# Optimization experiments

Hardware: AMD Instinct MI355X
Metric: run time of the kernel (lower is better)

The kernel has to match this reference:

```python
import jax, jax.numpy as jnp
import numpy as np

DK, DV, NH = 512, 256, 8  # matches init_kwargs


def rel_to_abs(x):
    # x: (B, N, L, 2L-1) -> (B, N, L, L) via pad/reshape trick
    B, N, L, _ = x.shape
    x = jnp.pad(x, ((0, 0), (0, 0), (0, 0), (0, 1)))          # (B,N,L,2L)
    x = x.reshape(B, N, L * 2 * L)
    x = jnp.pad(x, ((0, 0), (0, 0), (0, L - 1)))
    x = x.reshape(B, N, L + 1, 2 * L - 1)
    return x[:, :, :L, L - 1:]


def relative_logits_1d(q, rel_k):
    # q: (B, nh, A, Wd, dkh); rel_k: (dkh, 2*Wd-1)
    B, nh, A, Wd, _ = q.shape
    rel = jnp.einsum('bnawc,cm->bnawm', q, rel_k)             # (B,nh,A,Wd,2Wd-1)
    rel = rel.reshape(B, nh * A, Wd, 2 * Wd - 1)
    rel = rel_to_abs(rel).reshape(B, nh, A, 1, Wd, Wd)
    return jnp.broadcast_to(rel, (B, nh, A, A, Wd, Wd))


def reference(x, w_qkv, w_conv, w_out, key_rel_h, key_rel_w):
    B, Cin, H, W = x.shape
    dkh, dvh = DK // NH, DV // NH
    L = H * W
    # 1x1 qkv projection (stride 1)
    qkv = jnp.einsum('bchw,oc->bohw', x, w_qkv)               # (B, 2dk+dv, H, W)
    q = qkv[:, :DK]
    k = qkv[:, DK:2 * DK]
    v = qkv[:, 2 * DK:]
    flat_q = q.reshape(B, NH, dkh, L) * (dkh ** -0.5)
    flat_k = k.reshape(B, NH, dkh, L)
    flat_v = v.reshape(B, NH, dvh, L)
    logits = jnp.einsum('bncs,bnct->bnst', flat_q, flat_k)     # (B,nh,L,L)
    # relative position logits (uses the already-scaled q, as in the torch code)
    qr = flat_q.reshape(B, NH, dkh, H, W).transpose(0, 1, 3, 4, 2)  # (B,nh,H,W,dkh)
    w_rel = relative_logits_1d(qr, key_rel_w)                  # (B,nh,H,H,W,W)
    h_rel = relative_logits_1d(qr.transpose(0, 1, 3, 2, 4), key_rel_h)  # (B,nh,W,W,H,H)
    h_rel = h_rel.transpose(0, 1, 2, 4, 3, 5).reshape(B, NH, L, L)
    w_rel = w_rel.transpose(0, 1, 4, 2, 5, 3).reshape(B, NH, L, L)
    logits = logits + h_rel + w_rel
    weights = jax.nn.softmax(logits, axis=-1)
    attn = jnp.einsum('bnst,bnct->bnsc', weights, flat_v)      # (B,nh,L,dvh)
    attn = attn.transpose(0, 1, 3, 2).reshape(B, DV, H, W)
    attn = jnp.einsum('bchw,oc->bohw', attn, w_out)            # 1x1 out_proj
    conv_out = jax.lax.conv_general_dilated(
        x, w_conv, window_strides=(1, 1), padding=[(1, 1), (1, 1)],
        dimension_numbers=('NCHW', 'OIHW', 'NCHW'))            # (B, out_c-dv, H, W)
    return jnp.concatenate([conv_out, attn], axis=1)


def setup_inputs() -> dict:
    key = jax.random.key(0)
    ks = jax.random.split(key, 6)
    H, W, Cin = 32, 32, 256
    return {
        'x': jax.random.normal(ks[0], (8, Cin, H, W), jnp.float32),
        'w_qkv': jax.random.normal(ks[1], (2 * DK + DV, Cin), jnp.float32) * 0.02,
        'w_conv': jax.random.normal(ks[2], (256, Cin, 3, 3), jnp.float32) * 0.02,
        'w_out': jax.random.normal(ks[3], (DV, DV), jnp.float32) * 0.02,
        'key_rel_h': DK ** -0.5 + jax.random.normal(ks[4], (DK // NH, 2 * H - 1), jnp.float32),
        'key_rel_w': DK ** -0.5 + jax.random.normal(ks[5], (DK // NH, 2 * W - 1), jnp.float32),
    }
```

## Files before the change

kernel.cpp:

```cpp
#include <hip/hip_runtime.h>
#include <cstddef>
#include <cstdint>

#define NB 8
#define CIN 256
#define LL 1024
#define DKC 512
#define DVC 256
#define XPSTRIDE 295936

typedef short short8 __attribute__((ext_vector_type(8)));
typedef float f32x4 __attribute__((ext_vector_type(4)));

__device__ __forceinline__ unsigned short f2bf(float f) {
  unsigned int u = __float_as_uint(f);
  u += 0x7fffu + ((u >> 16) & 1u);
  return (unsigned short)(u >> 16);
}
__device__ __forceinline__ float bf2f(unsigned short u) {
  return __uint_as_float(((unsigned int)u) << 16);
}

__global__ __launch_bounds__(256) void prep_all(
    const float* __restrict__ x, const float* __restrict__ wconv,
    const float* __restrict__ wqkv, const float* __restrict__ wout,
    const float* __restrict__ krh, const float* __restrict__ krw,
    unsigned short* __restrict__ wtap, unsigned short* __restrict__ wqbf,
    unsigned short* __restrict__ woutbf, unsigned short* __restrict__ relTh,
    unsigned short* __restrict__ relTw, unsigned short* __restrict__ xTp) {
  __shared__ float tile[64][65];
  const int tid = threadIdx.x;
  if (blockIdx.x < 128) {
    const int st = blockIdx.x & 15;
    const int b = blockIdx.x >> 4;
    const int s0 = st * 64;
    const int h0 = st * 2;
    for (int cc = 0; cc < 4; ++cc) {
      const int c0 = cc * 64;
      {
        const int row = tid >> 2;
        const int j0 = (tid & 3) * 16;
#pragma unroll
        for (int k = 0; k < 4; ++k)
          *(float4*)&tile[row][j0 + k * 4] =
              *(const float4*)(x + ((size_t)(b * CIN + c0 + row)) * LL + s0 + j0 + k * 4);
      }
      __syncthreads();
      {
        const int sl = tid >> 2;
        const int cb = (tid & 3) * 16;
        unsigned short buf[16];
#pragma unroll
        for (int m = 0; m < 16; ++m) buf[m] = f2bf(tile[cb + m][sl]);
        const int hp = h0 + (sl >> 5) + 1;
        const int wp = (sl & 31) + 1;
        unsigned short* dst = xTp + (size_t)b * XPSTRIDE + (hp * 34 + wp) * 256 + c0 + cb;
        *(uint4*)dst = *(uint4*)&buf[0];
        *(uint4*)(dst + 8) = *(uint4*)&buf[8];
      }
      __syncthreads();
    }
    return;
  }
  const int idx = (blockIdx.x - 128) * 256 + tid;
  if (idx < 589824) {
    const int g = idx >> 14;
    const int ot = g / 9, tap = g - ot * 9;
    const int rem2 = idx & 16383;
    const int kc = rem2 >> 12;
    const int row = (rem2 >> 6) & 63, kin = rem2 & 63;
    const int o = ot * 64 + row, c = kc * 64 + kin;
    wtap[idx] = f2bf(wconv[(size_t)(o * 256 + c) * 9 + tap]);
  } else if (idx < 917504) {
    const int j = idx - 589824;
    const int g = j >> 12;
    const int ot = g >> 2, kc = g & 3;
    const int row = (j >> 6) & 63, kin = j & 63;
    const int o = ot * 64 + row, c = kc * 64 + kin;
    const float sc = (o < DKC) ? 0.125f * 1.44269504088896f : 1.0f;
    wqbf[j] = f2bf(wqkv[o * 256 + c] * sc);
  } else if (idx < 983040) {
    const int j = idx - 917504;
    const int g = j >> 12;
    const int o = (g >> 2) * 64 + ((j >> 6) & 63);
    const int c = (g & 3) * 64 + (j & 63);
    woutbf[j] = f2bf(wout[o * 256 + c]);
  } else if (idx < 991232) {
    const int j = idx - 983040;
    const int tbl = j >> 12;
    const int rest = j & 4095;
    const int m = rest >> 6, c = rest & 63;
    const float* src = tbl ? krw : krh;
    unsigned short* dst = tbl ? relTw : relTh;
    const float v = (m < 63) ? src[c * 63 + m] : 0.f;
    dst[m * 64 + c] = f2bf(v);
  } else {
    const int j2 = idx - 991232;
    const int b = j2 / 33792;
    const int rem = j2 - b * 33792;
    const int pos = rem >> 8, c = rem & 255;
    int hp, wp;
    if (pos < 34) { hp = 0; wp = pos; }
    else if (pos < 68) { hp = 33; wp = pos - 34; }
    else if (pos < 100) { hp = pos - 68 + 1; wp = 0; }
    else { hp = pos - 100 + 1; wp = 33; }
    xTp[(size_t)b * XPSTRIDE + (hp * 34 + wp) * 256 + c] = 0;
  }
}

__global__ __launch_bounds__(256) void qkv_mfma(
    const unsigned short* __restrict__ xTp, const unsigned short* __restrict__ wqbf,
    unsigned short* __restrict__ qbf, unsigned short* __restrict__ kbf,
    unsigned short* __restrict__ vbf) {
  __shared__ __align__(16) char qsmem[16640];
  unsigned short* bs = (unsigned short*)qsmem;
  float (*trans)[65] = (float(*)[65])qsmem;
  const int tid = threadIdx.x;
  const int lane = tid & 63, w = tid >> 6;
  const int n16 = lane & 15, quad = lane >> 4;
  const int ot = blockIdx.x;
  const int st = blockIdx.y;
  const int b = blockIdx.z;
  const int s0 = st * 64;
  const int h0 = st * 2;
  const int trow = tid >> 3, ck = tid & 7;

  const unsigned short* xb = xTp + (size_t)b * XPSTRIDE;
  const unsigned short* wA = wqbf + (size_t)ot * 16384 + (w * 16 + n16) * 64 + quad * 8;
  const int wpos = (trow & 31) + 1;

  f32x4 acc[4];
#pragma unroll
  for (int nt = 0; nt < 4; ++nt) acc[nt] = (f32x4){0.f, 0.f, 0.f, 0.f};

  uint4 rb0 = *(const uint4*)(xb + (size_t)((h0 + 1) * 34 + wpos) * 256 + ck * 8);
  uint4 rb1 = *(const uint4*)(xb + (size_t)((h0 + 2) * 34 + wpos) * 256 + ck * 8);
  short8 af0 = *(const short8*)(wA);
  short8 af1 = *(const short8*)(wA + 32);
#pragma unroll
  for (int kc = 0; kc < 4; ++kc) {
    __syncthreads();
    *(uint4*)&bs[trow * 64 + ((ck ^ (trow & 7)) * 8)] = rb0;
    *(uint4*)&bs[(trow + 32) * 64 + ((ck ^ (trow & 7)) * 8)] = rb1;
    __syncthreads();
    short8 a0 = af0, a1 = af1;
    if (kc < 3) {
      const int c0 = (kc + 1) * 64;
      rb0 = *(const uint4*)(xb + (size_t)((h0 + 1) * 34 + wpos) * 256 + c0 + ck * 8);
      rb1 = *(const uint4*)(xb + (size_t)((h0 + 2) * 34 + wpos) * 256 + c0 + ck * 8);
      af0 = *(const short8*)(wA + (kc + 1) * 4096);
      af1 = *(const short8*)(wA + (kc + 1) * 4096 + 32);
    }
#pragma unroll
    for (int nt = 0; nt < 4; ++nt) {
      short8 b0 = *(const short8*)&bs[(nt * 16 + n16) * 64 + ((quad ^ (n16 & 7)) * 8)];
      short8 b1 = *(const short8*)&bs[(nt * 16 + n16) * 64 + (((quad + 4) ^ (n16 & 7)) * 8)];
      acc[nt] = __builtin_amdgcn_mfma_f32_16x16x32_bf16(a0, b0, acc[nt], 0, 0, 0);
      acc[nt] = __builtin_amdgcn_mfma_f32_16x16x32_bf16(a1, b1, acc[nt], 0, 0, 0);
    }
  }
  __syncthreads();
#pragma unroll
  for (int nt = 0; nt < 4; ++nt)
#pragma unroll
    for (int reg = 0; reg < 4; ++reg)
      trans[w * 16 + quad * 4 + reg][nt * 16 + n16] = acc[nt][reg];
  __syncthreads();
  const int sl = tid >> 2;
  const int cseg = (tid & 3) * 16;
  unsigned short buf[16];
  if (ot < 16) {
#pragma unroll
    for (int m = 0; m < 16; ++m) buf[m] = f2bf(trans[cseg + m][sl]);
    unsigned short* dst;
    int head;
    if (ot < 8) { dst = qbf; head = ot; }
    else { dst = kbf; head = ot - 8; }
    const size_t base = (((size_t)(b * 8 + head)) * LL + s0 + sl) * 64 + cseg;
    *(uint4*)(dst + base) = *(uint4*)&buf[0];
    *(uint4*)(dst + base + 8) = *(uint4*)&buf[8];
  } else {
#pragma unroll
    for (int m = 0; m < 16; ++m) buf[m] = f2bf(trans[sl][cseg + m]);
    unsigned short* dst = vbf + ((size_t)b * DVC + (ot - 16) * 64 + sl) * LL + s0 + cseg;
    *(uint4*)dst = *(uint4*)&buf[0];
    *(uint4*)(dst + 8) = *(uint4*)&buf[8];
  }
}

__global__ __launch_bounds__(256) void conv_mfma(
    const unsigned short* __restrict__ xTp, const unsigned short* __restrict__ wtap,
    float* __restrict__ out) {
  __shared__ __align__(16) unsigned short bs[64 * 64];
  const int tid = threadIdx.x;
  const int lane = tid & 63, w = tid >> 6;
  const int n16 = lane & 15, quad = lane >> 4;
  const int ot = blockIdx.x;
  const int st = blockIdx.y;
  const int b = blockIdx.z;
  const int s0 = st * 64;
  const int h0 = st * 2;
  const int trow = tid >> 3;
  const int ck = tid & 7;

  const unsigned short* xb = xTp + (size_t)b * XPSTRIDE;
  const unsigned short* wA = wtap + (size_t)ot * 147456 + (w * 16 + n16) * 64 + quad * 8;

  f32x4 acc[4];
#pragma unroll
  for (int nt = 0; nt < 4; ++nt) acc[nt] = (f32x4){0.f, 0.f, 0.f, 0.f};

  uint4 rb0, rb1;
  auto loadB = [&](int it) {
    const int tap = it >> 2;
    const int c0 = (it & 3) * 64;
    const int dh = tap / 3 - 1;
    const int dw = tap - (tap / 3) * 3 - 1;
    const int wp = (trow & 31) + dw + 1;
    rb0 = *(const uint4*)(xb + (size_t)((h0 + dh + 1) * 34 + wp) * 256 + c0 + ck * 8);
    rb1 = *(const uint4*)(xb + (size_t)((h0 + dh + 2) * 34 + wp) * 256 + c0 + ck * 8);
  };
  loadB(0);
  short8 af0 = *(const short8*)(wA);
  short8 af1 = *(const short8*)(wA + 32);
  for (int it = 0; it < 36; ++it) {
    __syncthreads();
    *(uint4*)&bs[trow * 64 + ((ck ^ (trow & 7)) * 8)] = rb0;
    *(uint4*)&bs[(trow + 32) * 64 + ((ck ^ (trow & 7)) * 8)] = rb1;
    __syncthreads();
    short8 a0 = af0, a1 = af1;
    if (it < 35) {
      loadB(it + 1);
      af0 = *(const short8*)(wA + (size_t)(it + 1) * 4096);
      af1 = *(const short8*)(wA + (size_t)(it + 1) * 4096 + 32);
    }
#pragma unroll
    for (int nt = 0; nt < 4; ++nt) {
      short8 b0 = *(const short8*)&bs[(nt * 16 + n16) * 64 + ((quad ^ (n16 & 7)) * 8)];
      short8 b1 = *(const short8*)&bs[(nt * 16 + n16) * 64 + (((quad + 4) ^ (n16 & 7)) * 8)];
      acc[nt] = __builtin_amdgcn_mfma_f32_16x16x32_bf16(a0, b0, acc[nt], 0, 0, 0);
      acc[nt] = __builtin_amdgcn_mfma_f32_16x16x32_bf16(a1, b1, acc[nt], 0, 0, 0);
    }
  }
#pragma unroll
  for (int nt = 0; nt < 4; ++nt)
#pragma unroll
    for (int reg = 0; reg < 4; ++reg)
      out[((size_t)b * 512 + ot * 64 + w * 16 + quad * 4 + reg) * LL + s0 + nt * 16 + n16] =
          acc[nt][reg];
}

__global__ __launch_bounds__(256, 2) void attn_kernel(
    const unsigned short* __restrict__ qbf, const unsigned short* __restrict__ kbf,
    const unsigned short* __restrict__ vbf, const unsigned short* __restrict__ relTh,
    const unsigned short* __restrict__ relTw, unsigned short* __restrict__ abf) {
  __shared__ __align__(16) char smem[45056];
  unsigned short* ks = (unsigned short*)smem;
  unsigned short* vs = (unsigned short*)(smem + 8192);
  unsigned short* ps = (unsigned short*)(smem + 12288);
  unsigned short* rwtT = (unsigned short*)(smem + 28672);
  float* obuf = (float*)smem;

  const int tid = threadIdx.x;
  const int lane = tid & 63, w = tid >> 6;
  const int n16 = lane & 15, quad = lane >> 4;
  const int blk = blockIdx.x;
  const int bn = blk & 63, qt = blk >> 6;
  const int n = bn & 7, b = bn >> 3;
  const int s0 = qt * 128;
  const int pb = (w & 1) * 16;
  const int aar[2] = {4 * qt + (w >> 1), 4 * qt + 2 + (w >> 1)};

  const unsigned short* qbase = qbf + ((size_t)(b * 8 + n)) * LL * 64;
  const unsigned short* kbase = kbf + ((size_t)(b * 8 + n)) * LL * 64;
  const unsigned short* vbase = vbf + ((size_t)(b * 8 + n)) * 32 * LL;

  const int ck = tid & 7;
  const int trow = tid >> 3;

  uint4 pk0 = *(const uint4*)(kbase + trow * 64 + ck * 8);
  uint4 pk1 = *(const uint4*)(kbase + (trow + 32) * 64 + ck * 8);
  uint4 pv = *(const uint4*)(vbase + (size_t)trow * LL + ck * 8);

#pragma unroll
  for (int rs = 0; rs < 2; ++rs) {
    const int aa = aar[rs];
    const int sT = (pb + n16) * 32 + aa;
    short8 ra0 = *(const short8*)(qbase + (size_t)sT * 64 + quad * 8);
    short8 ra1 = *(const short8*)(qbase + (size_t)sT * 64 + 32 + quad * 8);
#pragma unroll
    for (int tbl = 0; tbl < 2; ++tbl) {
      const unsigned short* rel = tbl ? relTh : relTw;
      f32x4 acc[4];
#pragma unroll
      for (int mt = 0; mt < 4; ++mt) acc[mt] = (f32x4){0.f, 0.f, 0.f, 0.f};
#pragma unroll
      for (int mt = 0; mt < 4; ++mt) {
        short8 b0 = *(const short8*)(rel + (mt * 16 + n16) * 64 + quad * 8);
        short8 b1 = *(const short8*)(rel + (mt * 16 + n16) * 64 + 32 + quad * 8);
        acc[mt] = __builtin_amdgcn_mfma_f32_16x16x32_bf16(ra0, b0, acc[mt], 0, 0, 0);
        acc[mt] = __builtin_amdgcn_mfma_f32_16x16x32_bf16(ra1, b1, acc[mt], 0, 0, 0);
      }
      if (tbl == 0) {
#pragma unroll
        for (int mt = 0; mt < 4; ++mt)
#pragma unroll
          for (int reg = 0; reg < 4; ++reg)
            rwtT[(mt * 16 + n16) * 128 +
                 ((rs * 64 + w * 16 + quad * 4 + reg) ^ ((n16 & 7) * 8))] = f2bf(acc[mt][reg]);
      } else {
#pragma unroll
        for (int mt = 0; mt < 4; ++mt)
#pragma unroll
          for (int reg = 0; reg < 4; ++reg)
            ps[(rs * 64 + w * 16 + quad * 4 + reg) * 64 + mt * 16 + n16] = f2bf(acc[mt][reg]);
      }
    }
  }
  short8 qf[2][2];
#pragma unroll
  for (int rs = 0; rs < 2; ++rs) {
    const size_t qrow = (size_t)(s0 + rs * 64 + w * 16 + n16) * 64;
    qf[rs][0] = *(const short8*)(qbase + qrow + quad * 8);
    qf[rs][1] = *(const short8*)(qbase + qrow + 32 + quad * 8);
  }
  __syncthreads();
  float rhreg[2][2][4];
#pragma unroll
  for (int rs = 0; rs < 2; ++rs)
#pragma unroll
    for (int tt1 = 0; tt1 < 2; ++tt1)
#pragma unroll
      for (int reg = 0; reg < 4; ++reg) {
        const int iL = quad * 4 + reg;
        rhreg[rs][tt1][reg] =
            bf2f(ps[(rs * 64 + w * 16 + iL) * 64 + tt1 * 16 + n16 + 31 - pb - iL]);
      }

  float lacc[2][4] = {};
  f32x4 oacc[2][2];
#pragma unroll
  for (int rs = 0; rs < 2; ++rs)
#pragma unroll
    for (int ct = 0; ct < 2; ++ct) oacc[rs][ct] = (f32x4){0.f, 0.f, 0.f, 0.f};

  const int rbq = w * 16 + quad * 4;

  for (int kt64 = 0; kt64 < 16; ++kt64) {
    const int t0 = kt64 * 64;
    __syncthreads();
    *(uint4*)&ks[trow * 64 + ((ck ^ (trow & 7)) * 8)] = pk0;
    *(uint4*)&ks[(trow + 32) * 64 + ((ck ^ (trow & 7)) * 8)] = pk1;
    *(uint4*)&vs[trow * 64 + ((ck ^ (trow & 7)) * 8)] = pv;
    __syncthreads();
    if (kt64 < 15) {
      const unsigned short* kg = kbase + (size_t)(t0 + 64) * 64;
      pk0 = *(const uint4*)(kg + trow * 64 + ck * 8);
      pk1 = *(const uint4*)(kg + (trow + 32) * 64 + ck * 8);
      pv = *(const uint4*)(vbase + (size_t)trow * LL + t0 + 64 + ck * 8);
    }

    f32x4 sacc[2][4];
#pragma unroll
    for (int rs = 0; rs < 2; ++rs)
#pragma unroll
      for (int tt = 0; tt < 4; ++tt) sacc[rs][tt] = (f32x4){0.f, 0.f, 0.f, 0.f};
#pragma unroll
    for (int tt = 0; tt < 4; ++tt) {
      short8 kb0 = *(const short8*)&ks[(tt * 16 + n16) * 64 + ((quad ^ (n16 & 7)) * 8)];
      short8 kb1 = *(const short8*)&ks[(tt * 16 + n16) * 64 + (((quad + 4) ^ (n16 & 7)) * 8)];
#pragma unroll
      for (int rs = 0; rs < 2; ++rs) {
        sacc[rs][tt] = __builtin_amdgcn_mfma_f32_16x16x32_bf16(qf[rs][0], kb0, sacc[rs][tt], 0, 0, 0);
        sacc[rs][tt] = __builtin_amdgcn_mfma_f32_16x16x32_bf16(qf[rs][1], kb1, sacc[rs][tt], 0, 0, 0);
      }
    }
    float rwv[2][2][4];
#pragma unroll
    for (int rs = 0; rs < 2; ++rs)
#pragma unroll
      for (int h = 0; h < 2; ++h) {
        const int mw = (t0 >> 5) + h - aar[rs] + 31;
        const ushort4 rw4 =
            *(const ushort4*)&rwtT[mw * 128 + ((rs * 64 + rbq) ^ ((mw & 7) * 8))];
        rwv[rs][h][0] = bf2f(rw4.x); rwv[rs][h][1] = bf2f(rw4.y);
        rwv[rs][h][2] = bf2f(rw4.z); rwv[rs][h][3] = bf2f(rw4.w);
      }
#pragma unroll
    for (int rs = 0; rs < 2; ++rs)
#pragma unroll
      for (int tt = 0; tt < 4; ++tt)
#pragma unroll
        for (int reg = 0; reg < 4; ++reg) {
          const float e = __builtin_amdgcn_exp2f(sacc[rs][tt][reg] + rwv[rs][tt >> 1][reg] +
                                                 rhreg[rs][tt & 1][reg]);
          lacc[rs][reg] += e;
          const int r = quad * 4 + reg;
          ps[(rs * 64 + w * 16 + r) * 64 + (((tt * 2 + (n16 >> 3)) ^ (r & 7)) * 8) + (n16 & 7)] =
              (unsigned short)(__float_as_uint(e) >> 16);
        }
    __asm__ volatile("s_waitcnt lgkmcnt(0)" ::: "memory");
#pragma unroll
    for (int kt = 0; kt < 2; ++kt) {
      short8 pa[2];
#pragma unroll
      for (int rs = 0; rs < 2; ++rs)
        pa[rs] = *(const short8*)&ps[(rs * 64 + w * 16 + n16) * 64 +
                                     (((quad + 4 * kt) ^ (n16 & 7)) * 8)];
#pragma unroll
      for (int ct = 0; ct < 2; ++ct) {
        short8 vb = *(const short8*)&vs[(ct * 16 + n16) * 64 + (((quad + 4 * kt) ^ (n16 & 7)) * 8)];
#pragma unroll
        for (int rs = 0; rs < 2; ++rs)
          oacc[rs][ct] = __builtin_amdgcn_mfma_f32_16x16x32_bf16(pa[rs], vb, oacc[rs][ct], 0, 0, 0);
      }
    }
  }
  float linv[2][4];
#pragma unroll
  for (int rs = 0; rs < 2; ++rs)
#pragma unroll
    for (int reg = 0; reg < 4; ++reg) {
      float l = lacc[rs][reg];
#pragma unroll
      for (int m = 1; m < 16; m <<= 1) l += __shfl_xor(l, m, 16);
      linv[rs][reg] = 1.0f / l;
    }
  __syncthreads();
#pragma unroll
  for (int rs = 0; rs < 2; ++rs)
#pragma unroll
    for (int ct = 0; ct < 2; ++ct)
#pragma unroll
      for (int reg = 0; reg < 4; ++reg)
        obuf[(rs * 64 + w * 16 + quad * 4 + reg) * 33 + ct * 16 + n16] =
            oacc[rs][ct][reg] * linv[rs][reg];
  __syncthreads();
  {
    const int row = tid >> 1;
    const int cseg = (tid & 1) * 16;
    unsigned short buf16[16];
#pragma unroll
    for (int m = 0; m < 16; ++m) buf16[m] = f2bf(obuf[row * 33 + cseg + m]);
    unsigned short* dst = abf + (((size_t)b * LL) + s0 + row) * 256 + n * 32 + cseg;
    *(uint4*)dst = *(uint4*)&buf16[0];
    *(uint4*)(dst + 8) = *(uint4*)&buf16[8];
  }
}

__global__ __launch_bounds__(256) void proj_mfma(
    const unsigned short* __restrict__ abf, const unsigned short* __restrict__ woutbf,
    float* __restrict__ out) {
  __shared__ __align__(16) unsigned short bs[64 * 64];
  const int tid = threadIdx.x;
  const int lane = tid & 63, w = tid >> 6;
  const int n16 = lane & 15, quad = lane >> 4;
  const int ot = blockIdx.x;
  const int st = blockIdx.y;
  const int b = blockIdx.z;
  const int s0 = st * 64;
  const int trow = tid >> 3, ck = tid & 7;

  const unsigned short* ab = abf + ((size_t)b * LL + s0) * 256;
  const unsigned short* wA = woutbf + (size_t)ot * 16384 + (w * 16 + n16) * 64 + quad * 8;

  f32x4 acc[4];
#pragma unroll
  for (int nt = 0; nt < 4; ++nt) acc[nt] = (f32x4){0.f, 0.f, 0.f, 0.f};

  uint4 rb0 = *(const uint4*)(ab + (size_t)trow * 256 + ck * 8);
  uint4 rb1 = *(const uint4*)(ab + (size_t)(trow + 32) * 256 + ck * 8);
  short8 af0 = *(const short8*)(wA);
  short8 af1 = *(const short8*)(wA + 32);
#pragma unroll
  for (int kc = 0; kc < 4; ++kc) {
    __syncthreads();
    *(uint4*)&bs[trow * 64 + ((ck ^ (trow & 7)) * 8)] = rb0;
    *(uint4*)&bs[(trow + 32) * 64 + ((ck ^ (trow & 7)) * 8)] = rb1;
    __syncthreads();
    short8 a0 = af0, a1 = af1;
    if (kc < 3) {
      const int c0 = (kc + 1) * 64;
      rb0 = *(const uint4*)(ab + (size_t)trow * 256 + c0 + ck * 8);
      rb1 = *(const uint4*)(ab + (size_t)(trow + 32) * 256 + c0 + ck * 8);
      af0 = *(const short8*)(wA + (kc + 1) * 4096);
      af1 = *(const short8*)(wA + (kc + 1) * 4096 + 32);
    }
#pragma unroll
    for (int nt = 0; nt < 4; ++nt) {
      short8 b0 = *(const short8*)&bs[(nt * 16 + n16) * 64 + ((quad ^ (n16 & 7)) * 8)];
      short8 b1 = *(const short8*)&bs[(nt * 16 + n16) * 64 + (((quad + 4) ^ (n16 & 7)) * 8)];
      acc[nt] = __builtin_amdgcn_mfma_f32_16x16x32_bf16(a0, b0, acc[nt], 0, 0, 0);
      acc[nt] = __builtin_amdgcn_mfma_f32_16x16x32_bf16(a1, b1, acc[nt], 0, 0, 0);
    }
  }
#pragma unroll
  for (int nt = 0; nt < 4; ++nt)
#pragma unroll
    for (int reg = 0; reg < 4; ++reg)
      out[((size_t)b * 512 + 256 + ot * 64 + w * 16 + quad * 4 + reg) * LL + s0 + nt * 16 + n16] =
          acc[nt][reg];
}

extern "C" void kernel_launch(void* const* d_in, const int* in_sizes, int n_in,
                              void* d_out, int out_size, void* d_ws, size_t ws_size,
                              hipStream_t stream) {
  const float* x     = (const float*)d_in[0];
  const float* wqkv  = (const float*)d_in[1];
  const float* wconv = (const float*)d_in[2];
  const float* wout  = (const float*)d_in[3];
  const float* krh   = (const float*)d_in[4];
  const float* krw   = (const float*)d_in[5];
  float* out = (float*)d_out;

  unsigned short* qbf = (unsigned short*)d_ws;
  unsigned short* kbf = qbf + (size_t)NB * 8 * LL * 64;
  unsigned short* vbf = kbf + (size_t)NB * 8 * LL * 64;
  unsigned short* abf = vbf + (size_t)NB * DVC * LL;
  unsigned short* relTh = abf + (size_t)NB * LL * DVC;
  unsigned short* relTw = relTh + 4096;
  unsigned short* xTp = relTw + 4096;
  unsigned short* wtap = xTp + (size_t)NB * XPSTRIDE;
  unsigned short* wqbf = wtap + 589824;
  unsigned short* woutbf = wqbf + 327680;

  prep_all<<<dim3(5056), 256, 0, stream>>>(x, wconv, wqkv, wout, krh, krw,
                                           wtap, wqbf, woutbf, relTh, relTw, xTp);
  qkv_mfma<<<dim3(20, 16, NB), 256, 0, stream>>>(xTp, wqbf, qbf, kbf, vbf);
  conv_mfma<<<dim3(4, 16, NB), 256, 0, stream>>>(xTp, wtap, out);
  attn_kernel<<<dim3(512), 256, 0, stream>>>(qbf, kbf, vbf, relTh, relTw, abf);
  proj_mfma<<<dim3(4, 16, NB), 256, 0, stream>>>(abf, woutbf, out);
}
```

Before: 161.8 us.

## Load GEMM B fragments directly from global into registers, drop LDS staging

In the qkv, conv and output-projection MFMA kernels, each lane now loads its B-operand fragments straight from global memory into registers, double-buffered across k-steps. This replaces the shared-memory tile and the two barriers per iteration. The aim is to remove LDS traffic and synchronisation so loads overlap with MFMAs. In exchange, each of the four waves fetches the same B data on its own, which raises global/L2 traffic fourfold and raises register pressure, especially in the fully unrolled 36-step conv loop.

```diff
diff --git a/kernel.cpp b/kernel.cpp
--- a/kernel.cpp
+++ b/kernel.cpp
@@ -112,9 +112,7 @@
     const unsigned short* __restrict__ xTp, const unsigned short* __restrict__ wqbf,
     unsigned short* __restrict__ qbf, unsigned short* __restrict__ kbf,
     unsigned short* __restrict__ vbf) {
-  __shared__ __align__(16) char qsmem[16640];
-  unsigned short* bs = (unsigned short*)qsmem;
-  float (*trans)[65] = (float(*)[65])qsmem;
+  __shared__ float trans[64][65];
   const int tid = threadIdx.x;
   const int lane = tid & 63, w = tid >> 6;
   const int n16 = lane & 15, quad = lane >> 4;
@@ -123,43 +121,51 @@
   const int b = blockIdx.z;
   const int s0 = st * 64;
   const int h0 = st * 2;
-  const int trow = tid >> 3, ck = tid & 7;
 
   const unsigned short* xb = xTp + (size_t)b * XPSTRIDE;
   const unsigned short* wA = wqbf + (size_t)ot * 16384 + (w * 16 + n16) * 64 + quad * 8;
-  const int wpos = (trow & 31) + 1;
+
+  const unsigned short* bp[4];
+#pragma unroll
+  for (int nt = 0; nt < 4; ++nt) {
+    const int sl2 = nt * 16 + n16;
+    const int hp = h0 + (sl2 >> 5) + 1;
+    const int wp = (sl2 & 31) + 1;
+    bp[nt] = xb + (size_t)(hp * 34 + wp) * 256 + quad * 8;
+  }
 
   f32x4 acc[4];
 #pragma unroll
   for (int nt = 0; nt < 4; ++nt) acc[nt] = (f32x4){0.f, 0.f, 0.f, 0.f};
 
-  uint4 rb0 = *(const uint4*)(xb + (size_t)((h0 + 1) * 34 + wpos) * 256 + ck * 8);
-  uint4 rb1 = *(const uint4*)(xb + (size_t)((h0 + 2) * 34 + wpos) * 256 + ck * 8);
-  short8 af0 = *(const short8*)(wA);
-  short8 af1 = *(const short8*)(wA + 32);
+  short8 bf[2][4][2];
+  short8 af[2][2];
+#pragma unroll
+  for (int nt = 0; nt < 4; ++nt) {
+    bf[0][nt][0] = *(const short8*)(bp[nt]);
+    bf[0][nt][1] = *(const short8*)(bp[nt] + 32);
+  }
+  af[0][0] = *(const short8*)(wA);
+  af[0][1] = *(const short8*)(wA + 32);
 #pragma unroll
   for (int kc = 0; kc < 4; ++kc) {
-    __syncthreads();
-    *(uint4*)&bs[trow * 64 + ((ck ^ (trow & 7)) * 8)] = rb0;
-    *(uint4*)&bs[(trow + 32) * 64 + ((ck ^ (trow & 7)) * 8)] = rb1;
-    __syncthreads();
-    short8 a0 = af0, a1 = af1;
+    const int cur = kc & 1, nxt = cur ^ 1;
     if (kc < 3) {
       const int c0 = (kc + 1) * 64;
-      rb0 = *(const uint4*)(xb + (size_t)((h0 + 1) * 34 + wpos) * 256 + c0 + ck * 8);
-      rb1 = *(const uint4*)(xb + (size_t)((h0 + 2) * 34 + wpos) * 256 + c0 + ck * 8);
-      af0 = *(const short8*)(wA + (kc + 1) * 4096);
-      af1 = *(const short8*)(wA + (kc + 1) * 4096 + 32);
+#pragma unroll
+      for (int nt = 0; nt < 4; ++nt) {
+        bf[nxt][nt][0] = *(const short8*)(bp[nt] + c0);
+        bf[nxt][nt][1] = *(const short8*)(bp[nt] + c0 + 32);
+      }
+      af[nxt][0] = *(const short8*)(wA + (kc + 1) * 4096);
+      af[nxt][1] = *(const short8*)(wA + (kc + 1) * 4096 + 32);
     }
 #pragma unroll
     for (int nt = 0; nt < 4; ++nt) {
-      short8 b0 = *(const short8*)&bs[(nt * 16 + n16) * 64 + ((quad ^ (n16 & 7)) * 8)];
-      short8 b1 = *(const short8*)&bs[(nt * 16 + n16) * 64 + (((quad + 4) ^ (n16 & 7)) * 8)];
-      acc[nt] = __builtin_amdgcn_mfma_f32_16x16x32_bf16(a0, b0, acc[nt], 0, 0, 0);
-      acc[nt] = __builtin_amdgcn_mfma_f32_16x16x32_bf16(a1, b1, acc[nt], 0, 0, 0);
-    }
-  }
-  __syncthreads();
+      acc[nt] = __builtin_amdgcn_mfma_f32_16x16x32_bf16(af[cur][0], bf[cur][nt][0], acc[nt], 0, 0, 0);
+      acc[nt] = __builtin_amdgcn_mfma_f32_16x16x32_bf16(af[cur][1], bf[cur][nt][1], acc[nt], 0, 0, 0);
+    }
+  }
 #pragma unroll
   for (int nt = 0; nt < 4; ++nt)
 #pragma unroll
@@ -191,7 +197,6 @@
 __global__ __launch_bounds__(256) void conv_mfma(
     const unsigned short* __restrict__ xTp, const unsigned short* __restrict__ wtap,
     float* __restrict__ out) {
-  __shared__ __align__(16) unsigned short bs[64 * 64];
   const int tid = threadIdx.x;
   const int lane = tid & 63, w = tid >> 6;
   const int n16 = lane & 15, quad = lane >> 4;
@@ -200,46 +205,57 @@
   const int b = blockIdx.z;
   const int s0 = st * 64;
   const int h0 = st * 2;
-  const int trow = tid >> 3;
-  const int ck = tid & 7;
 
   const unsigned short* xb = xTp + (size_t)b * XPSTRIDE;
   const unsigned short* wA = wtap + (size_t)ot * 147456 + (w * 16 + n16) * 64 + quad * 8;
 
+  const unsigned short* bp[4];
+#pragma unroll
+  for (int nt = 0; nt < 4; ++nt) {
+    const int sl2 = nt * 16 + n16;
+    const int hp = h0 + (sl2 >> 5);
+    const int wp = (sl2 & 31);
+    bp[nt] = xb + (size_t)(hp * 34 + wp) * 256 + quad * 8;
+  }
+
   f32x4 acc[4];
 #pragma unroll
   for (int nt = 0; nt < 4; ++nt) acc[nt] = (f32x4){0.f, 0.f, 0.f, 0.f};
 
-  uint4 rb0, rb1;
-  auto loadB = [&](int it) {
+  short8 bf[2][4][2];
+  short8 af[2][2];
+  auto boff = [](int it) -> int {
     const int tap = it >> 2;
-    const int c0 = (it & 3) * 64;
-    const int dh = tap / 3 - 1;
-    const int dw = tap - (tap / 3) * 3 - 1;
-    const int wp = (trow & 31) + dw + 1;
-    rb0 = *(const uint4*)(xb + (size_t)((h0 + dh + 1) * 34 + wp) * 256 + c0 + ck * 8);
-    rb1 = *(const uint4*)(xb + (size_t)((h0 + dh + 2) * 34 + wp) * 256 + c0 + ck * 8);
+    const int dh = tap / 3, dw = tap - (tap / 3) * 3;
+    return (dh * 34 + dw) * 256 + (it & 3) * 64;
   };
-  loadB(0);
-  short8 af0 = *(const short8*)(wA);
-  short8 af1 = *(const short8*)(wA + 32);
+  {
+    const int o0 = boff(0);
+#pragma unroll
+    for (int nt = 0; nt < 4; ++nt) {
+      bf[0][nt][0] = *(const short8*)(bp[nt] + o0);
+      bf[0][nt][1] = *(const short8*)(bp[nt] + o0 + 32);
+    }
+    af[0][0] = *(const short8*)(wA);
+    af[0][1] = *(const short8*)(wA + 32);
+  }
+#pragma unroll
   for (int it = 0; it < 36; ++it) {
-    __syncthreads();
-    *(uint4*)&bs[trow * 64 + ((ck ^ (trow & 7)) * 8)] = rb0;
-    *(uint4*)&bs[(trow + 32) * 64 + ((ck ^ (trow & 7)) * 8)] = rb1;
-    __syncthreads();
-    short8 a0 = af0, a1 = af1;
+    const int cur = it & 1, nxt = cur ^ 1;
     if (it < 35) {
-      loadB(it + 1);
-      af0 = *(const short8*)(wA + (size_t)(it + 1) * 4096);
-      af1 = *(const short8*)(wA + (size_t)(it + 1) * 4096 + 32);
+      const int o1 = boff(it + 1);
+#pragma unroll
+      for (int nt = 0; nt < 4; ++nt) {
+        bf[nxt][nt][0] = *(const short8*)(bp[nt] + o1);
+        bf[nxt][nt][1] = *(const short8*)(bp[nt] + o1 + 32);
+      }
+      af[nxt][0] = *(const short8*)(wA + (size_t)(it + 1) * 4096);
+      af[nxt][1] = *(const short8*)(wA + (size_t)(it + 1) * 4096 + 32);
     }
 #pragma unroll
     for (int nt = 0; nt < 4; ++nt) {
-      short8 b0 = *(const short8*)&bs[(nt * 16 + n16) * 64 + ((quad ^ (n16 & 7)) * 8)];
-      short8 b1 = *(const short8*)&bs[(nt * 16 + n16) * 64 + (((quad + 4) ^ (n16 & 7)) * 8)];
-      acc[nt] = __builtin_amdgcn_mfma_f32_16x16x32_bf16(a0, b0, acc[nt], 0, 0, 0);
-      acc[nt] = __builtin_amdgcn_mfma_f32_16x16x32_bf16(a1, b1, acc[nt], 0, 0, 0);
+      acc[nt] = __builtin_amdgcn_mfma_f32_16x16x32_bf16(af[cur][0], bf[cur][nt][0], acc[nt], 0, 0, 0);
+      acc[nt] = __builtin_amdgcn_mfma_f32_16x16x32_bf16(af[cur][1], bf[cur][nt][1], acc[nt], 0, 0, 0);
     }
   }
 #pragma unroll
@@ -451,7 +467,6 @@
 __global__ __launch_bounds__(256) void proj_mfma(
     const unsigned short* __restrict__ abf, const unsigned short* __restrict__ woutbf,
     float* __restrict__ out) {
-  __shared__ __align__(16) unsigned short bs[64 * 64];
   const int tid = threadIdx.x;
   const int lane = tid & 63, w = tid >> 6;
   const int n16 = lane & 15, quad = lane >> 4;
@@ -459,39 +474,45 @@
   const int st = blockIdx.y;
   const int b = blockIdx.z;
   const int s0 = st * 64;
-  const int trow = tid >> 3, ck = tid & 7;
 
   const unsigned short* ab = abf + ((size_t)b * LL + s0) * 256;
   const unsigned short* wA = woutbf + (size_t)ot * 16384 + (w * 16 + n16) * 64 + quad * 8;
 
+  const unsigned short* bp[4];
+#pragma unroll
+  for (int nt = 0; nt < 4; ++nt)
+    bp[nt] = ab + (size_t)(nt * 16 + n16) * 256 + quad * 8;
+
   f32x4 acc[4];
 #pragma unroll
   for (int nt = 0; nt < 4; ++nt) acc[nt] = (f32x4){0.f, 0.f, 0.f, 0.f};
 
-  uint4 rb0 = *(const uint4*)(ab + (size_t)trow * 256 + ck * 8);
-  uint4 rb1 = *(const uint4*)(ab + (size_t)(trow + 32) * 256 + ck * 8);
-  short8 af0 = *(const short8*)(wA);
-  short8 af1 = *(const short8*)(wA + 32);
+  short8 bf[2][4][2];
+  short8 af[2][2];
+#pragma unroll
+  for (int nt = 0; nt < 4; ++nt) {
+    bf[0][nt][0] = *(const short8*)(bp[nt]);
+    bf[0][nt][1] = *(const short8*)(bp[nt] + 32);
+  }
+  af[0][0] = *(const short8*)(wA);
+  af[0][1] = *(const short8*)(wA + 32);
 #pragma unroll
   for (int kc = 0; kc < 4; ++kc) {
-    __syncthreads();
-    *(uint4*)&bs[trow * 64 + ((ck ^ (trow & 7)) * 8)] = rb0;
-    *(uint4*)&bs[(trow + 32) * 64 + ((ck ^ (trow & 7)) * 8)] = rb1;
-    __syncthreads();
-    short8 a0 = af0, a1 = af1;
+    const int cur = kc & 1, nxt = cur ^ 1;
     if (kc < 3) {
       const int c0 = (kc + 1) * 64;
-      rb0 = *(const uint4*)(ab + (size_t)trow * 256 + c0 + ck * 8);
-      rb1 = *(const uint4*)(ab + (size_t)(trow + 32) * 256 + c0 + ck * 8);
-      af0 = *(const short8*)(wA + (kc + 1) * 4096);
-      af1 = *(const short8*)(wA + (kc + 1) * 4096 + 32);
+#pragma unroll
+      for (int nt = 0; nt < 4; ++nt) {
+        bf[nxt][nt][0] = *(const short8*)(bp[nt] + c0);
+        bf[nxt][nt][1] = *(const short8*)(bp[nt] + c0 + 32);
+      }
+      af[nxt][0] = *(const short8*)(wA + (kc + 1) * 4096);
+      af[nxt][1] = *(const short8*)(wA + (kc + 1) * 4096 + 32);
     }
 #pragma unroll
     for (int nt = 0; nt < 4; ++nt) {
-      short8 b0 = *(const short8*)&bs[(nt * 16 + n16) * 64 + ((quad ^ (n16 & 7)) * 8)];
-      short8 b1 = *(const short8*)&bs[(nt * 16 + n16) * 64 + (((quad + 4) ^ (n16 & 7)) * 8)];
-      acc[nt] = __builtin_amdgcn_mfma_f32_16x16x32_bf16(a0, b0, acc[nt], 0, 0, 0);
-      acc[nt] = __builtin_amdgcn_mfma_f32_16x16x32_bf16(a1, b1, acc[nt], 0, 0, 0);
+      acc[nt] = __builtin_amdgcn_mfma_f32_16x16x32_bf16(af[cur][0], bf[cur][nt][0], acc[nt], 0, 0, 0);
+      acc[nt] = __builtin_amdgcn_mfma_f32_16x16x32_bf16(af[cur][1], bf[cur][nt][1], acc[nt], 0, 0, 0);
     }
   }
 #pragma unroll
```

New measurement: 254.6 us. 57.4% more time.
